# Performance work log

Hardware: AMD Instinct MI355X
Metric: run time of the kernel (lower is better)

The kernel has to match this reference:

```python
import jax, jax.numpy as jnp
import numpy as np

# Production-scale dims: b=8, t=1024, emb=1024, heads=16 -> head dim s=64.
B, T, E, H = 8, 1024, 1024, 16
S = E // H  # 64, per-head dim; tokeys/toqueries/tovalues are Linear(S, S) shared across heads


def setup_inputs() -> dict:
    key = jax.random.key(0)
    k0, k1, k2, k3, k4, k5 = jax.random.split(key, 6)
    return {
        "x": jax.random.normal(k0, (B, T, E), dtype=jnp.float32),
        # full lengths: keeps the length-mask path live without all--inf rows (NaN softmax)
        "lengths": jnp.full((B,), T, dtype=jnp.int32),
        # torch Linear stores weight as (out_features, in_features); y = x @ W.T
        "Wk": jax.random.normal(k1, (S, S), dtype=jnp.float32) / np.float32(np.sqrt(S)),
        "Wq": jax.random.normal(k2, (S, S), dtype=jnp.float32) / np.float32(np.sqrt(S)),
        "Wv": jax.random.normal(k3, (S, S), dtype=jnp.float32) / np.float32(np.sqrt(S)),
        "Wu": jax.random.normal(k4, (E, E), dtype=jnp.float32) / np.float32(np.sqrt(E)),
        "bu": jax.random.normal(k5, (E,), dtype=jnp.float32) * jnp.float32(0.02),
    }


def reference(x, lengths, Wk, Wq, Wv, Wu, bu):
    b, t, e = x.shape
    h = H
    s = e // h
    xh = x.reshape(b, t, h, s)

    # per-head projections (same S x S weight for every head), torch Linear: x @ W.T
    queries = jnp.einsum('bths,os->btho', xh, Wq)
    keys = jnp.einsum('bths,os->btho', xh, Wk)
    values = jnp.einsum('bths,os->btho', xh, Wv)

    # scale q and k each by e**-0.25 (net 1/sqrt(e) on scores)
    scale = jnp.float32(e) ** jnp.float32(-0.25)
    dot = jnp.einsum('bqho,bkho->bhqk', queries * scale, keys * scale)  # (b,h,t,t)

    # causal mask (mask_diagonal=False -> strictly upper triangle masked)
    i = jnp.arange(t)[:, None]
    j = jnp.arange(t)[None, :]
    causal = j <= i  # (t,t)
    # length mask over key positions: key index k < lengths[b]
    lenmask = jnp.arange(t)[None, :] < lengths[:, None]  # (b,t)
    valid = causal[None, None, :, :] & lenmask[:, None, None, :]  # (b,1->h,t,t)

    dot = jnp.where(valid, dot, -jnp.inf)
    attn = jax.nn.softmax(dot, axis=-1)

    out = jnp.einsum('bhqk,bkho->bqho', attn, values).reshape(b, t, e)
    return jnp.einsum('bte,oe->bto', out, Wu) + bu
```

## Files before the change

### kernel.cpp

```cpp
#include <hip/hip_runtime.h>
#include <stdint.h>

#define B_ 8
#define T_ 1024
#define E_ 1024
#define H_ 16
#define S_ 64

typedef __attribute__((ext_vector_type(8))) short bf16x8;
typedef __attribute__((ext_vector_type(4))) short bf16x4;
typedef __attribute__((ext_vector_type(4))) float f32x4;

__device__ __forceinline__ f32x4 mfma_pv(bf16x4 a, bf16x4 b, f32x4 c) {
  return __builtin_amdgcn_mfma_f32_16x16x16bf16_1k(a, b, c, 0, 0, 0);
}

__device__ __forceinline__ float e2(float x) { return __builtin_amdgcn_exp2f(x); }

__device__ __forceinline__ ushort f2bf(float f) {
  union { float f; uint32_t u; } v; v.f = f;
  uint32_t r = (v.u + 0x7FFFu + ((v.u >> 16) & 1u)) >> 16;
  return (ushort)r;
}
__device__ __forceinline__ float bf2f(ushort u) {
  union { uint32_t u; float f; } v; v.u = ((uint32_t)u) << 16;
  return v.f;
}

__device__ __forceinline__ uint32_t pk2(float a, float b) {
  return __builtin_amdgcn_perm(__float_as_uint(b) + 0x8000u,
                               __float_as_uint(a) + 0x8000u, 0x07060302u);
}
__device__ __forceinline__ bf16x4 pack4(const float* p) {
  union { uint32_t u[2]; bf16x4 v; } pu;
  pu.u[0] = pk2(p[0], p[1]);
  pu.u[1] = pk2(p[2], p[3]);
  return pu.v;
}

__device__ __forceinline__ void gload_lds16(const ushort* g, ushort* l) {
  __builtin_amdgcn_global_load_lds(
      (const __attribute__((address_space(1))) uint32_t*)g,
      (__attribute__((address_space(3))) uint32_t*)l, 16, 0, 0);
}

__device__ __forceinline__ bf16x8 load8(const void* p, size_t idx, bool isf32) {
  if (isf32) {
    const float* fp = (const float*)p + idx;
    f32x4 f0 = *(const f32x4*)(fp);
    f32x4 f1 = *(const f32x4*)(fp + 4);
    bf16x8 r;
    #pragma unroll
    for (int i = 0; i < 4; ++i) r[i] = (short)f2bf(f0[i]);
    #pragma unroll
    for (int i = 0; i < 4; ++i) r[4 + i] = (short)f2bf(f1[i]);
    return r;
  }
  return *(const bf16x8*)((const ushort*)p + idx);
}

__device__ __forceinline__ bool detect_f32_wave(const uint32_t* __restrict__ x) {
  const int lane = threadIdx.x & 63;
  int sane = 0;
  #pragma unroll
  for (int j = 0; j < 4; ++j) {
    uint32_t lo = x[lane * 4 + j] & 0xFFFFu;
    uint32_t e = (lo >> 7) & 0xFFu;
    sane += (e >= 96u && e <= 158u) ? 1 : 0;
  }
  #pragma unroll
  for (int off = 32; off >= 1; off >>= 1) sane += __shfl_xor(sane, off);
  return sane < 192;
}

__global__ __launch_bounds__(256) void cvt_kernel(
    const void* __restrict__ x,
    const void* __restrict__ Wu, const void* __restrict__ bu,
    const void* __restrict__ Wq, const void* __restrict__ Wk,
    const void* __restrict__ Wv,
    ushort* __restrict__ wub, ushort* __restrict__ bub,
    ushort* __restrict__ wqkv) {
  const bool f32 = detect_f32_wave((const uint32_t*)x);
  if (blockIdx.x < 512) {
    size_t base = (size_t)blockIdx.x * 2048 + threadIdx.x * 8;
    *(bf16x8*)(wub + base) = load8(Wu, base, f32);
  } else if (blockIdx.x == 512) {
    if (threadIdx.x < 128) {
      size_t base = (size_t)threadIdx.x * 8;
      *(bf16x8*)(bub + base) = load8(bu, base, f32);
    }
  } else {
    const void* Ws[3] = {Wq, Wk, Wv};
    int idx = blockIdx.x - 513;
    int w = idx >> 1, half = idx & 1;
    size_t base = (size_t)half * 2048 + threadIdx.x * 8;
    *(bf16x8*)(wqkv + w * 4096 + base) = load8(Ws[w], base, f32);
  }
}

#define QSCALE 0.045084220f

__global__ __launch_bounds__(256) void qkv_kernel(
    const void* __restrict__ x, const ushort* __restrict__ wqkv,
    ushort* __restrict__ qb, ushort* __restrict__ kb, ushort* __restrict__ vb) {
  __shared__ ushort qs[64 * 72];
  __shared__ ushort ks[64 * 72];
  __shared__ ushort vs[64 * 72];
  const bool f32 = detect_f32_wave((const uint32_t*)x);
  const int tid = threadIdx.x;
  const int lane = tid & 63, wave = tid >> 6;
  const int m = lane & 15, quad = lane >> 4;
  const int tile = blockIdx.x & 15;
  const int h = (blockIdx.x >> 4) & 15;
  const int b = blockIdx.x >> 8;
  const int t0 = tile * 64;

  const size_t xrow = ((size_t)b * T_ + t0 + wave * 16 + m) * E_ + h * S_;
  bf16x8 a0 = load8(x, xrow + quad * 8, f32);
  bf16x8 a1 = load8(x, xrow + 32 + quad * 8, f32);

  #pragma unroll
  for (int w = 0; w < 3; ++w) {
    const float sc = (w == 0) ? QSCALE : 1.0f;
    ushort* dst = (w == 0) ? qs : (w == 1) ? ks : vs;
    #pragma unroll
    for (int nt = 0; nt < 4; ++nt) {
      const ushort* wrow = wqkv + w * 4096 + (nt * 16 + m) * S_;
      bf16x8 b0 = *(const bf16x8*)(wrow + quad * 8);
      bf16x8 b1 = *(const bf16x8*)(wrow + 32 + quad * 8);
      f32x4 acc = {0.f, 0.f, 0.f, 0.f};
      acc = __builtin_amdgcn_mfma_f32_16x16x32_bf16(a0, b0, acc, 0, 0, 0);
      acc = __builtin_amdgcn_mfma_f32_16x16x32_bf16(a1, b1, acc, 0, 0, 0);
      #pragma unroll
      for (int i = 0; i < 4; ++i) {
        int lr = wave * 16 + quad * 4 + i;
        int o  = nt * 16 + m;
        if (w == 2) {
          vs[o * 72 + lr] = f2bf(acc[i]);
        } else {
          dst[lr * 72 + o] = f2bf(acc[i] * sc);
        }
      }
    }
  }

  __syncthreads();

  const int row = tid >> 2, ck = (tid & 3) * 16;
  const size_t qkbase = (((size_t)b * H_ + h) * T_ + t0 + row) * S_ + ck;
  *(bf16x8*)(qb + qkbase)     = *(const bf16x8*)(qs + row * 72 + ck);
  *(bf16x8*)(qb + qkbase + 8) = *(const bf16x8*)(qs + row * 72 + ck + 8);
  *(bf16x8*)(kb + qkbase)     = *(const bf16x8*)(ks + row * 72 + ck);
  *(bf16x8*)(kb + qkbase + 8) = *(const bf16x8*)(ks + row * 72 + ck + 8);
  const size_t vbase = (((size_t)b * H_ + h) * S_ + row) * T_ + t0 + ck;
  *(bf16x8*)(vb + vbase)      = *(const bf16x8*)(vs + row * 72 + ck);
  *(bf16x8*)(vb + vbase + 8)  = *(const bf16x8*)(vs + row * 72 + ck + 8);
}

__global__ __launch_bounds__(256) void attn_kernel(
    const ushort* __restrict__ qb, const ushort* __restrict__ kb,
    const ushort* __restrict__ vb, const int* __restrict__ lengths,
    ushort* __restrict__ ao) {
  __shared__ ushort klds[2][64 * 64];
  __shared__ ushort vlds[2][64 * 64];

  const int tid = threadIdx.x;
  const int lane = tid & 63, wave = tid >> 6;
  const int m = lane & 15, quad = lane >> 4;
  const int pr = blockIdx.x >> 7;
  const int bh = blockIdx.x & 127;
  const int b  = bh >> 4, h = bh & 15;
  const int qtA = pr, qtB = 15 - pr;
  const int len = lengths[b];

  const size_t head_off = ((size_t)b * H_ + h) * (size_t)T_ * S_;
  const ushort* Q  = qb + head_off;
  const ushort* K  = kb + head_off;
  const ushort* Vt = vb + head_off;

  const int sr  = lane >> 3;
  const int ssw = 8 * ((lane & 7) ^ sr);

  const int qwA = qtA * 64 + wave * 16;
  const int qwB = qtB * 64 + wave * 16;
  bf16x8 aqA0 = *(const bf16x8*)(Q + (size_t)(qwA + m) * S_ + quad * 8);
  bf16x8 aqA1 = *(const bf16x8*)(Q + (size_t)(qwA + m) * S_ + 32 + quad * 8);
  bf16x8 aqB0 = *(const bf16x8*)(Q + (size_t)(qwB + m) * S_ + quad * 8);
  bf16x8 aqB1 = *(const bf16x8*)(Q + (size_t)(qwB + m) * S_ + 32 + quad * 8);

  const int qminA = min(qwA + m, len - 1);
  const int qminB = min(qwB + m, len - 1);

  f32x4 oA[4], oB[4], LaccA, LaccB;
  #pragma unroll
  for (int i = 0; i < 4; ++i) {
    oA[i] = (f32x4){0.f, 0.f, 0.f, 0.f};
    oB[i] = (f32x4){0.f, 0.f, 0.f, 0.f};
  }
  LaccA = (f32x4){0.f, 0.f, 0.f, 0.f};
  LaccB = (f32x4){0.f, 0.f, 0.f, 0.f};

  bf16x4 ones;
  #pragma unroll
  for (int i = 0; i < 4; ++i) ones[i] = (short)0x3F80;

  #pragma unroll
  for (int p = 0; p < 2; ++p) {
    const int wrow = wave * 16 + p * 8;
    gload_lds16(K  + (size_t)(wrow + sr) * S_ + ssw, &klds[0][wrow * 64]);
    gload_lds16(Vt + (size_t)(wrow + sr) * T_ + ssw, &vlds[0][wrow * 64]);
  }
  __syncthreads();

  const int swzr = 8 * (m & 7);

  for (int kt = 0; kt <= qtB; ++kt) {
    const bool doA = (kt <= qtA);
    const bool mA = (kt == qtA) || ((kt + 1) * 64 > len);
    const bool mB = (kt == qtB) || ((kt + 1) * 64 > len);

    if (kt < qtB) {
      const ushort* Kn = K + (size_t)(kt + 1) * 64 * S_;
      #pragma unroll
      for (int p = 0; p < 2; ++p) {
        const int wrow = wave * 16 + p * 8;
        gload_lds16(Kn + (size_t)(wrow + sr) * S_ + ssw,
                    &klds[(kt + 1) & 1][wrow * 64]);
        gload_lds16(Vt + (size_t)(wrow + sr) * T_ + (kt + 1) * 64 + ssw,
                    &vlds[(kt + 1) & 1][wrow * 64]);
      }
    }

    const ushort* kls = klds[kt & 1];
    const ushort* vls = vlds[kt & 1];

    bf16x4 vv[4][4];
    #pragma unroll
    for (int nt = 0; nt < 4; ++nt) {
      #pragma unroll
      for (int v4 = 0; v4 < 4; ++v4) {
        vv[nt][v4] = *(const bf16x4*)(vls + (v4 * 16 + m) * 64 +
                                      8 * ((2 * nt + (quad >> 1)) ^ (m & 7)) +
                                      (quad & 1) * 4);
      }
    }

    bf16x4 pfA[4], pfB[4];
    #pragma unroll
    for (int nt = 0; nt < 4; ++nt) {
      const ushort* krow = kls + (nt * 16 + m) * 64;
      bf16x8 ak0 = *(const bf16x8*)(krow + ((8 * quad) ^ swzr));
      bf16x8 ak1 = *(const bf16x8*)(krow + ((32 + 8 * quad) ^ swzr));
      const int kl0 = kt * 64 + nt * 16 + quad * 4;

      __builtin_amdgcn_s_setprio(1);
      f32x4 sB = {0.f, 0.f, 0.f, 0.f};
      sB = __builtin_amdgcn_mfma_f32_16x16x32_bf16(ak0, aqB0, sB, 0, 0, 0);
      sB = __builtin_amdgcn_mfma_f32_16x16x32_bf16(ak1, aqB1, sB, 0, 0, 0);
      f32x4 sA = {0.f, 0.f, 0.f, 0.f};
      if (doA) {
        sA = __builtin_amdgcn_mfma_f32_16x16x32_bf16(ak0, aqA0, sA, 0, 0, 0);
        sA = __builtin_amdgcn_mfma_f32_16x16x32_bf16(ak1, aqA1, sA, 0, 0, 0);
      }
      __builtin_amdgcn_s_setprio(0);

      float pB[4];
      #pragma unroll
      for (int i = 0; i < 4; ++i) {
        float s = sB[i];
        if (mB) s = (kl0 + i <= qminB) ? s : -1e30f;
        pB[i] = e2(s);
      }
      pfB[nt] = pack4(pB);

      if (doA) {
        float pA[4];
        #pragma unroll
        for (int i = 0; i < 4; ++i) {
          float s = sA[i];
          if (mA) s = (kl0 + i <= qminA) ? s : -1e30f;
          pA[i] = e2(s);
        }
        pfA[nt] = pack4(pA);
      }
    }

    __builtin_amdgcn_s_setprio(1);
    #pragma unroll
    for (int nt = 0; nt < 4; ++nt) {
      LaccB = mfma_pv(pfB[nt], ones, LaccB);
      if (doA) LaccA = mfma_pv(pfA[nt], ones, LaccA);
      #pragma unroll
      for (int v4 = 0; v4 < 4; ++v4) {
        oB[v4] = mfma_pv(pfB[nt], vv[nt][v4], oB[v4]);
        if (doA) oA[v4] = mfma_pv(pfA[nt], vv[nt][v4], oA[v4]);
      }
    }
    __builtin_amdgcn_s_setprio(0);

    if (kt < qtB) __syncthreads();
  }

  #pragma unroll
  for (int i = 0; i < 4; ++i) {
    float ilA = (LaccA[i] > 0.f) ? 1.0f / LaccA[i] : 0.f;
    float ilB = (LaccB[i] > 0.f) ? 1.0f / LaccB[i] : 0.f;
    size_t baseA = ((size_t)b * T_ + qwA + quad * 4 + i) * E_ + h * 64;
    size_t baseB = ((size_t)b * T_ + qwB + quad * 4 + i) * E_ + h * 64;
    #pragma unroll
    for (int v4 = 0; v4 < 4; ++v4) {
      ao[baseA + v4 * 16 + m] = f2bf(oA[v4][i] * ilA);
      ao[baseB + v4 * 16 + m] = f2bf(oB[v4][i] * ilB);
    }
  }
}

__global__ __launch_bounds__(256) void proj_kernel(
    const ushort* __restrict__ A, const ushort* __restrict__ Wu,
    const ushort* __restrict__ bu, float* __restrict__ Y) {
  __shared__ ushort As[128 * 72];
  __shared__ ushort Bs[128 * 72];
  const int tid = threadIdx.x;
  const int lane = tid & 63, wave = tid >> 6;
  const int m = lane & 15, quad = lane >> 4;
  const int m0 = blockIdx.x * 128, n0 = blockIdx.y * 128;
  const int wm = (wave & 1) * 64, wn = (wave >> 1) * 64;

  f32x4 acc[4][4];
  #pragma unroll
  for (int i = 0; i < 4; ++i)
    #pragma unroll
    for (int j = 0; j < 4; ++j) acc[i][j] = (f32x4){0.f, 0.f, 0.f, 0.f};

  bf16x8 pa[4], pb[4];
  #pragma unroll
  for (int p = 0; p < 4; ++p) {
    int c = tid + p * 256;
    int row = c >> 3, col = (c & 7) * 8;
    pa[p] = *(const bf16x8*)(A + (size_t)(m0 + row) * E_ + col);
    pb[p] = *(const bf16x8*)(Wu + (size_t)(n0 + row) * E_ + col);
  }

  for (int k0 = 0; k0 < E_; k0 += 64) {
    __syncthreads();
    #pragma unroll
    for (int p = 0; p < 4; ++p) {
      int c = tid + p * 256;
      int row = c >> 3, col = (c & 7) * 8;
      *(bf16x8*)(As + row * 72 + col) = pa[p];
      *(bf16x8*)(Bs + row * 72 + col) = pb[p];
    }
    __syncthreads();

    if (k0 + 64 < E_) {
      #pragma unroll
      for (int p = 0; p < 4; ++p) {
        int c = tid + p * 256;
        int row = c >> 3, col = (c & 7) * 8;
        pa[p] = *(const bf16x8*)(A + (size_t)(m0 + row) * E_ + k0 + 64 + col);
        pb[p] = *(const bf16x8*)(Wu + (size_t)(n0 + row) * E_ + k0 + 64 + col);
      }
    }

    #pragma unroll
    for (int kk = 0; kk < 64; kk += 32) {
      bf16x8 af[4], bfrag[4];
      #pragma unroll
      for (int i = 0; i < 4; ++i)
        af[i] = *(const bf16x8*)(As + (wm + i * 16 + m) * 72 + kk + quad * 8);
      #pragma unroll
      for (int j = 0; j < 4; ++j)
        bfrag[j] = *(const bf16x8*)(Bs + (wn + j * 16 + m) * 72 + kk + quad * 8);
      #pragma unroll
      for (int i = 0; i < 4; ++i)
        #pragma unroll
        for (int j = 0; j < 4; ++j)
          acc[i][j] = __builtin_amdgcn_mfma_f32_16x16x32_bf16(af[i], bfrag[j], acc[i][j], 0, 0, 0);
    }
  }

  #pragma unroll
  for (int j = 0; j < 4; ++j) {
    float bias = bf2f(bu[n0 + wn + j * 16 + m]);
    #pragma unroll
    for (int i = 0; i < 4; ++i) {
      #pragma unroll
      for (int r = 0; r < 4; ++r) {
        int grow = m0 + wm + i * 16 + quad * 4 + r;
        int gcol = n0 + wn + j * 16 + m;
        Y[(size_t)grow * E_ + gcol] = acc[i][j][r] + bias;
      }
    }
  }
}

extern "C" void kernel_launch(void* const* d_in, const int* in_sizes, int n_in,
                              void* d_out, int out_size, void* d_ws, size_t ws_size,
                              hipStream_t stream) {
  const void* x  = d_in[0];
  const int* lengths = (const int*)d_in[1];
  const void* Wk = d_in[2];
  const void* Wq = d_in[3];
  const void* Wv = d_in[4];
  const void* Wu = d_in[5];
  const void* bu = d_in[6];
  float* out = (float*)d_out;

  const size_t hsz = (size_t)B_ * H_ * T_ * S_;
  ushort* qb   = (ushort*)d_ws;
  ushort* kb   = qb + hsz;
  ushort* vb   = kb + hsz;
  ushort* ao   = vb + hsz;
  ushort* wub  = ao + hsz;
  ushort* bub  = wub + (size_t)E_ * E_;
  ushort* wqkv = bub + E_;

  cvt_kernel<<<dim3(519), dim3(256), 0, stream>>>(x, Wu, bu, Wq, Wk, Wv, wub, bub, wqkv);
  qkv_kernel<<<dim3(B_ * H_ * (T_ / 64)), dim3(256), 0, stream>>>(x, wqkv, qb, kb, vb);
  attn_kernel<<<dim3(B_ * H_ * 8), dim3(256), 0, stream>>>(qb, kb, vb, lengths, ao);
  proj_kernel<<<dim3((B_ * T_) / 128, E_ / 128), dim3(256), 0, stream>>>(ao, wub, bub, out);
}
```

Baseline: 211.7 us.

## Prefetch V tiles into double-buffered registers and interleave QK with PV

```diff
diff --git a/kernel.cpp b/kernel.cpp
--- a/kernel.cpp
+++ b/kernel.cpp
@@ -157,12 +157,99 @@
   *(bf16x8*)(vb + vbase + 8)  = *(const bf16x8*)(vs + row * 72 + ck + 8);
 }
 
-__global__ __launch_bounds__(256) void attn_kernel(
+__device__ __forceinline__ void attn_iter(
+    int kt, int qtA, int qtB, int len, int m, int quad, int wave,
+    int sr, int ssw, int swzr, int qminA, int qminB,
+    const ushort* __restrict__ K, const ushort* __restrict__ vbase,
+    const ushort* kread, ushort* kwrite,
+    bf16x8 aqA0, bf16x8 aqA1, bf16x8 aqB0, bf16x8 aqB1,
+    bf16x4 (&vcur)[4][4], bf16x4 (&vnext)[4][4],
+    f32x4 (&oA)[4], f32x4 (&oB)[4], f32x4& LaccA, f32x4& LaccB,
+    bf16x4 ones) {
+  const bool doA = (kt <= qtA);
+  const bool mA = (kt == qtA) || ((kt + 1) * 64 > len);
+  const bool mB = (kt == qtB) || ((kt + 1) * 64 > len);
+  const bool notlast = (kt < qtB);
+
+  if (notlast) {
+    const ushort* Kn = K + (size_t)(kt + 1) * 64 * S_;
+    #pragma unroll
+    for (int p = 0; p < 2; ++p) {
+      const int wrow = wave * 16 + p * 8;
+      gload_lds16(Kn + (size_t)(wrow + sr) * S_ + ssw, kwrite + wrow * 64);
+    }
+    const ushort* vb1 = vbase + (kt + 1) * 64;
+    #pragma unroll
+    for (int v4 = 0; v4 < 4; ++v4) {
+      #pragma unroll
+      for (int nt = 0; nt < 4; ++nt) {
+        vnext[nt][v4] = *(const bf16x4*)(vb1 + (size_t)(v4 * 16) * T_ + nt * 16);
+      }
+    }
+  }
+
+  #pragma unroll
+  for (int nt = 0; nt < 4; ++nt) {
+    const ushort* krow = kread + (nt * 16 + m) * 64;
+    bf16x8 ak0 = *(const bf16x8*)(krow + ((8 * quad) ^ swzr));
+    bf16x8 ak1 = *(const bf16x8*)(krow + ((32 + 8 * quad) ^ swzr));
+    const int kl0 = kt * 64 + nt * 16 + quad * 4;
+
+    __builtin_amdgcn_s_setprio(1);
+    f32x4 sB = {0.f, 0.f, 0.f, 0.f};
+    sB = __builtin_amdgcn_mfma_f32_16x16x32_bf16(ak0, aqB0, sB, 0, 0, 0);
+    sB = __builtin_amdgcn_mfma_f32_16x16x32_bf16(ak1, aqB1, sB, 0, 0, 0);
+    f32x4 sA = {0.f, 0.f, 0.f, 0.f};
+    if (doA) {
+      sA = __builtin_amdgcn_mfma_f32_16x16x32_bf16(ak0, aqA0, sA, 0, 0, 0);
+      sA = __builtin_amdgcn_mfma_f32_16x16x32_bf16(ak1, aqA1, sA, 0, 0, 0);
+    }
+    __builtin_amdgcn_s_setprio(0);
+
+    float pB[4];
+    #pragma unroll
+    for (int i = 0; i < 4; ++i) {
+      float s = sB[i];
+      if (mB) s = (kl0 + i <= qminB) ? s : -1e30f;
+      pB[i] = e2(s);
+    }
+    bf16x4 pfB = pack4(pB);
+    bf16x4 pfA;
+    if (doA) {
+      float pA[4];
+      #pragma unroll
+      for (int i = 0; i < 4; ++i) {
+        float s = sA[i];
+        if (mA) s = (kl0 + i <= qminA) ? s : -1e30f;
+        pA[i] = e2(s);
+      }
+      pfA = pack4(pA);
+    }
+
+    __builtin_amdgcn_s_setprio(1);
+    LaccB = mfma_pv(pfB, ones, LaccB);
+    if (doA) LaccA = mfma_pv(pfA, ones, LaccA);
+    #pragma unroll
+    for (int v4 = 0; v4 < 4; ++v4) {
+      oB[v4] = mfma_pv(pfB, vcur[nt][v4], oB[v4]);
+      if (doA) oA[v4] = mfma_pv(pfA, vcur[nt][v4], oA[v4]);
+    }
+    __builtin_amdgcn_s_setprio(0);
+  }
+
+  if (notlast) {
+    asm volatile("s_waitcnt vmcnt(16)" ::: "memory");
+    __builtin_amdgcn_sched_barrier(0);
+    __builtin_amdgcn_s_barrier();
+    __builtin_amdgcn_sched_barrier(0);
+  }
+}
+
+__global__ __launch_bounds__(256, 3) void attn_kernel(
     const ushort* __restrict__ qb, const ushort* __restrict__ kb,
     const ushort* __restrict__ vb, const int* __restrict__ lengths,
     ushort* __restrict__ ao) {
   __shared__ ushort klds[2][64 * 64];
-  __shared__ ushort vlds[2][64 * 64];
 
   const int tid = threadIdx.x;
   const int lane = tid & 63, wave = tid >> 6;
@@ -180,6 +267,7 @@
 
   const int sr  = lane >> 3;
   const int ssw = 8 * ((lane & 7) ^ sr);
+  const int swzr = 8 * (m & 7);
 
   const int qwA = qtA * 64 + wave * 16;
   const int qwB = qtB * 64 + wave * 16;
@@ -191,6 +279,8 @@
   const int qminA = min(qwA + m, len - 1);
   const int qminB = min(qwB + m, len - 1);
 
+  const ushort* vbase = Vt + (size_t)m * T_ + quad * 4;
+
   f32x4 oA[4], oB[4], LaccA, LaccB;
   #pragma unroll
   for (int i = 0; i < 4; ++i) {
@@ -204,101 +294,33 @@
   #pragma unroll
   for (int i = 0; i < 4; ++i) ones[i] = (short)0x3F80;
 
+  bf16x4 vvA[4][4], vvB[4][4];
+
   #pragma unroll
   for (int p = 0; p < 2; ++p) {
     const int wrow = wave * 16 + p * 8;
-    gload_lds16(K  + (size_t)(wrow + sr) * S_ + ssw, &klds[0][wrow * 64]);
-    gload_lds16(Vt + (size_t)(wrow + sr) * T_ + ssw, &vlds[0][wrow * 64]);
-  }
-  __syncthreads();
-
-  const int swzr = 8 * (m & 7);
-
-  for (int kt = 0; kt <= qtB; ++kt) {
-    const bool doA = (kt <= qtA);
-    const bool mA = (kt == qtA) || ((kt + 1) * 64 > len);
-    const bool mB = (kt == qtB) || ((kt + 1) * 64 > len);
-
-    if (kt < qtB) {
-      const ushort* Kn = K + (size_t)(kt + 1) * 64 * S_;
-      #pragma unroll
-      for (int p = 0; p < 2; ++p) {
-        const int wrow = wave * 16 + p * 8;
-        gload_lds16(Kn + (size_t)(wrow + sr) * S_ + ssw,
-                    &klds[(kt + 1) & 1][wrow * 64]);
-        gload_lds16(Vt + (size_t)(wrow + sr) * T_ + (kt + 1) * 64 + ssw,
-                    &vlds[(kt + 1) & 1][wrow * 64]);
-      }
-    }
-
-    const ushort* kls = klds[kt & 1];
-    const ushort* vls = vlds[kt & 1];
-
-    bf16x4 vv[4][4];
+    gload_lds16(K + (size_t)(wrow + sr) * S_ + ssw, &klds[0][wrow * 64]);
+  }
+  #pragma unroll
+  for (int v4 = 0; v4 < 4; ++v4) {
     #pragma unroll
     for (int nt = 0; nt < 4; ++nt) {
-      #pragma unroll
-      for (int v4 = 0; v4 < 4; ++v4) {
-        vv[nt][v4] = *(const bf16x4*)(vls + (v4 * 16 + m) * 64 +
-                                      8 * ((2 * nt + (quad >> 1)) ^ (m & 7)) +
-                                      (quad & 1) * 4);
-      }
-    }
-
-    bf16x4 pfA[4], pfB[4];
-    #pragma unroll
-    for (int nt = 0; nt < 4; ++nt) {
-      const ushort* krow = kls + (nt * 16 + m) * 64;
-      bf16x8 ak0 = *(const bf16x8*)(krow + ((8 * quad) ^ swzr));
-      bf16x8 ak1 = *(const bf16x8*)(krow + ((32 + 8 * quad) ^ swzr));
-      const int kl0 = kt * 64 + nt * 16 + quad * 4;
-
-      __builtin_amdgcn_s_setprio(1);
-      f32x4 sB = {0.f, 0.f, 0.f, 0.f};
-      sB = __builtin_amdgcn_mfma_f32_16x16x32_bf16(ak0, aqB0, sB, 0, 0, 0);
-      sB = __builtin_amdgcn_mfma_f32_16x16x32_bf16(ak1, aqB1, sB, 0, 0, 0);
-      f32x4 sA = {0.f, 0.f, 0.f, 0.f};
-      if (doA) {
-        sA = __builtin_amdgcn_mfma_f32_16x16x32_bf16(ak0, aqA0, sA, 0, 0, 0);
-        sA = __builtin_amdgcn_mfma_f32_16x16x32_bf16(ak1, aqA1, sA, 0, 0, 0);
-      }
-      __builtin_amdgcn_s_setprio(0);
-
-      float pB[4];
-      #pragma unroll
-      for (int i = 0; i < 4; ++i) {
-        float s = sB[i];
-        if (mB) s = (kl0 + i <= qminB) ? s : -1e30f;
-        pB[i] = e2(s);
-      }
-      pfB[nt] = pack4(pB);
-
-      if (doA) {
-        float pA[4];
-        #pragma unroll
-        for (int i = 0; i < 4; ++i) {
-          float s = sA[i];
-          if (mA) s = (kl0 + i <= qminA) ? s : -1e30f;
-          pA[i] = e2(s);
-        }
-        pfA[nt] = pack4(pA);
-      }
-    }
-
-    __builtin_amdgcn_s_setprio(1);
-    #pragma unroll
-    for (int nt = 0; nt < 4; ++nt) {
-      LaccB = mfma_pv(pfB[nt], ones, LaccB);
-      if (doA) LaccA = mfma_pv(pfA[nt], ones, LaccA);
-      #pragma unroll
-      for (int v4 = 0; v4 < 4; ++v4) {
-        oB[v4] = mfma_pv(pfB[nt], vv[nt][v4], oB[v4]);
-        if (doA) oA[v4] = mfma_pv(pfA[nt], vv[nt][v4], oA[v4]);
-      }
-    }
-    __builtin_amdgcn_s_setprio(0);
-
-    if (kt < qtB) __syncthreads();
+      vvA[nt][v4] = *(const bf16x4*)(vbase + (size_t)(v4 * 16) * T_ + nt * 16);
+    }
+  }
+  asm volatile("s_waitcnt vmcnt(16)" ::: "memory");
+  __builtin_amdgcn_sched_barrier(0);
+  __builtin_amdgcn_s_barrier();
+  __builtin_amdgcn_sched_barrier(0);
+
+  for (int kt = 0; kt <= qtB; kt += 2) {
+    attn_iter(kt, qtA, qtB, len, m, quad, wave, sr, ssw, swzr, qminA, qminB,
+              K, vbase, klds[0], klds[1], aqA0, aqA1, aqB0, aqB1,
+              vvA, vvB, oA, oB, LaccA, LaccB, ones);
+    if (kt + 1 <= qtB)
+      attn_iter(kt + 1, qtA, qtB, len, m, quad, wave, sr, ssw, swzr, qminA, qminB,
+                K, vbase, klds[1], klds[0], aqA0, aqA1, aqB0, aqB1,
+                vvB, vvA, oA, oB, LaccA, LaccB, ones);
   }
 
   #pragma unroll
```

After: 369.6 us. 74.6% more time.

## Split paired causal query tiles into one tile per block, heaviest first

Applied to the files above, without the earlier changes.

```diff
diff --git a/kernel.cpp b/kernel.cpp
--- a/kernel.cpp
+++ b/kernel.cpp
@@ -157,7 +157,7 @@
   *(bf16x8*)(vb + vbase + 8)  = *(const bf16x8*)(vs + row * 72 + ck + 8);
 }
 
-__global__ __launch_bounds__(256) void attn_kernel(
+__global__ __launch_bounds__(256, 3) void attn_kernel(
     const ushort* __restrict__ qb, const ushort* __restrict__ kb,
     const ushort* __restrict__ vb, const int* __restrict__ lengths,
     ushort* __restrict__ ao) {
@@ -167,10 +167,10 @@
   const int tid = threadIdx.x;
   const int lane = tid & 63, wave = tid >> 6;
   const int m = lane & 15, quad = lane >> 4;
-  const int pr = blockIdx.x >> 7;
+  const int ord = blockIdx.x >> 7;
   const int bh = blockIdx.x & 127;
   const int b  = bh >> 4, h = bh & 15;
-  const int qtA = pr, qtB = 15 - pr;
+  const int qt = 15 - ord;
   const int len = lengths[b];
 
   const size_t head_off = ((size_t)b * H_ + h) * (size_t)T_ * S_;
@@ -180,25 +180,18 @@
 
   const int sr  = lane >> 3;
   const int ssw = 8 * ((lane & 7) ^ sr);
-
-  const int qwA = qtA * 64 + wave * 16;
-  const int qwB = qtB * 64 + wave * 16;
-  bf16x8 aqA0 = *(const bf16x8*)(Q + (size_t)(qwA + m) * S_ + quad * 8);
-  bf16x8 aqA1 = *(const bf16x8*)(Q + (size_t)(qwA + m) * S_ + 32 + quad * 8);
-  bf16x8 aqB0 = *(const bf16x8*)(Q + (size_t)(qwB + m) * S_ + quad * 8);
-  bf16x8 aqB1 = *(const bf16x8*)(Q + (size_t)(qwB + m) * S_ + 32 + quad * 8);
-
-  const int qminA = min(qwA + m, len - 1);
-  const int qminB = min(qwB + m, len - 1);
-
-  f32x4 oA[4], oB[4], LaccA, LaccB;
-  #pragma unroll
-  for (int i = 0; i < 4; ++i) {
-    oA[i] = (f32x4){0.f, 0.f, 0.f, 0.f};
-    oB[i] = (f32x4){0.f, 0.f, 0.f, 0.f};
-  }
-  LaccA = (f32x4){0.f, 0.f, 0.f, 0.f};
-  LaccB = (f32x4){0.f, 0.f, 0.f, 0.f};
+  const int swzr = 8 * (m & 7);
+
+  const int qw = qt * 64 + wave * 16;
+  bf16x8 aq0 = *(const bf16x8*)(Q + (size_t)(qw + m) * S_ + quad * 8);
+  bf16x8 aq1 = *(const bf16x8*)(Q + (size_t)(qw + m) * S_ + 32 + quad * 8);
+
+  const int qmin = min(qw + m, len - 1);
+
+  f32x4 o[4], Lacc;
+  #pragma unroll
+  for (int i = 0; i < 4; ++i) o[i] = (f32x4){0.f, 0.f, 0.f, 0.f};
+  Lacc = (f32x4){0.f, 0.f, 0.f, 0.f};
 
   bf16x4 ones;
   #pragma unroll
@@ -212,14 +205,10 @@
   }
   __syncthreads();
 
-  const int swzr = 8 * (m & 7);
-
-  for (int kt = 0; kt <= qtB; ++kt) {
-    const bool doA = (kt <= qtA);
-    const bool mA = (kt == qtA) || ((kt + 1) * 64 > len);
-    const bool mB = (kt == qtB) || ((kt + 1) * 64 > len);
-
-    if (kt < qtB) {
+  for (int kt = 0; kt <= qt; ++kt) {
+    const bool msk = (kt == qt) || ((kt + 1) * 64 > len);
+
+    if (kt < qt) {
       const ushort* Kn = K + (size_t)(kt + 1) * 64 * S_;
       #pragma unroll
       for (int p = 0; p < 2; ++p) {
@@ -245,7 +234,7 @@
       }
     }
 
-    bf16x4 pfA[4], pfB[4];
+    bf16x4 pf[4];
     #pragma unroll
     for (int nt = 0; nt < 4; ++nt) {
       const ushort* krow = kls + (nt * 16 + m) * 64;
@@ -254,64 +243,41 @@
       const int kl0 = kt * 64 + nt * 16 + quad * 4;
 
       __builtin_amdgcn_s_setprio(1);
-      f32x4 sB = {0.f, 0.f, 0.f, 0.f};
-      sB = __builtin_amdgcn_mfma_f32_16x16x32_bf16(ak0, aqB0, sB, 0, 0, 0);
-      sB = __builtin_amdgcn_mfma_f32_16x16x32_bf16(ak1, aqB1, sB, 0, 0, 0);
-      f32x4 sA = {0.f, 0.f, 0.f, 0.f};
-      if (doA) {
-        sA = __builtin_amdgcn_mfma_f32_16x16x32_bf16(ak0, aqA0, sA, 0, 0, 0);
-        sA = __builtin_amdgcn_mfma_f32_16x16x32_bf16(ak1, aqA1, sA, 0, 0, 0);
-      }
+      f32x4 s4 = {0.f, 0.f, 0.f, 0.f};
+      s4 = __builtin_amdgcn_mfma_f32_16x16x32_bf16(ak0, aq0, s4, 0, 0, 0);
+      s4 = __builtin_amdgcn_mfma_f32_16x16x32_bf16(ak1, aq1, s4, 0, 0, 0);
       __builtin_amdgcn_s_setprio(0);
 
-      float pB[4];
+      float p4[4];
       #pragma unroll
       for (int i = 0; i < 4; ++i) {
-        float s = sB[i];
-        if (mB) s = (kl0 + i <= qminB) ? s : -1e30f;
-        pB[i] = e2(s);
-      }
-      pfB[nt] = pack4(pB);
-
-      if (doA) {
-        float pA[4];
-        #pragma unroll
-        for (int i = 0; i < 4; ++i) {
-          float s = sA[i];
-          if (mA) s = (kl0 + i <= qminA) ? s : -1e30f;
-          pA[i] = e2(s);
-        }
-        pfA[nt] = pack4(pA);
-      }
+        float s = s4[i];
+        if (msk) s = (kl0 + i <= qmin) ? s : -1e30f;
+        p4[i] = e2(s);
+      }
+      pf[nt] = pack4(p4);
     }
 
     __builtin_amdgcn_s_setprio(1);
     #pragma unroll
     for (int nt = 0; nt < 4; ++nt) {
-      LaccB = mfma_pv(pfB[nt], ones, LaccB);
-      if (doA) LaccA = mfma_pv(pfA[nt], ones, LaccA);
-      #pragma unroll
-      for (int v4 = 0; v4 < 4; ++v4) {
-        oB[v4] = mfma_pv(pfB[nt], vv[nt][v4], oB[v4]);
-        if (doA) oA[v4] = mfma_pv(pfA[nt], vv[nt][v4], oA[v4]);
-      }
+      Lacc = mfma_pv(pf[nt], ones, Lacc);
+      #pragma unroll
+      for (int v4 = 0; v4 < 4; ++v4)
+        o[v4] = mfma_pv(pf[nt], vv[nt][v4], o[v4]);
     }
     __builtin_amdgcn_s_setprio(0);
 
-    if (kt < qtB) __syncthreads();
+    if (kt < qt) __syncthreads();
   }
 
   #pragma unroll
   for (int i = 0; i < 4; ++i) {
-    float ilA = (LaccA[i] > 0.f) ? 1.0f / LaccA[i] : 0.f;
-    float ilB = (LaccB[i] > 0.f) ? 1.0f / LaccB[i] : 0.f;
-    size_t baseA = ((size_t)b * T_ + qwA + quad * 4 + i) * E_ + h * 64;
-    size_t baseB = ((size_t)b * T_ + qwB + quad * 4 + i) * E_ + h * 64;
-    #pragma unroll
-    for (int v4 = 0; v4 < 4; ++v4) {
-      ao[baseA + v4 * 16 + m] = f2bf(oA[v4][i] * ilA);
-      ao[baseB + v4 * 16 + m] = f2bf(oB[v4][i] * ilB);
-    }
+    float il = (Lacc[i] > 0.f) ? 1.0f / Lacc[i] : 0.f;
+    size_t base = ((size_t)b * T_ + qw + quad * 4 + i) * E_ + h * 64;
+    #pragma unroll
+    for (int v4 = 0; v4 < 4; ++v4)
+      ao[base + v4 * 16 + m] = f2bf(o[v4][i] * il);
   }
 }
 
@@ -417,6 +383,6 @@
 
   cvt_kernel<<<dim3(519), dim3(256), 0, stream>>>(x, Wu, bu, Wq, Wk, Wv, wub, bub, wqkv);
   qkv_kernel<<<dim3(B_ * H_ * (T_ / 64)), dim3(256), 0, stream>>>(x, wqkv, qb, kb, vb);
-  attn_kernel<<<dim3(B_ * H_ * 8), dim3(256), 0, stream>>>(qb, kb, vb, lengths, ao);
+  attn_kernel<<<dim3(B_ * H_ * 16), dim3(256), 0, stream>>>(qb, kb, vb, lengths, ao);
   proj_kernel<<<dim3((B_ * T_) / 128, E_ / 128), dim3(256), 0, stream>>>(ao, wub, bub, out);
 }
```

After: 183.1 us. 13.5% less time.
